# Kernel tuning notes

Measured on AMD Instinct MI355X. Metric: run time of the kernel, lower is better.

The kernel has to match this reference:

```python
import jax, jax.numpy as jnp
import numpy as np

ANCHORS = jnp.array([[0.57273, 0.677385], [1.87446, 2.06253], [3.33843, 5.47434],
                     [7.88282, 3.52778], [9.77052, 9.16828]], dtype=jnp.float32)
IOU_THR = 0.6
SCALE_NOOBJ = 1.0
SCALE_OBJ = 5.0
DS = 32.0          # downsample_rate
EPS = 1e-7


def _iou_wh(w1, h1, w2, h2):
    # GetCenterAlignIouBetween: boxes aligned at centers -> IoU depends on w,h only
    inter = jnp.minimum(w1, w2) * jnp.minimum(h1, h2)
    return inter / (w1 * h1 + w2 * h2 - inter + EPS)


def setup_inputs() -> dict:
    B, W, H, A, C, M = 128, 19, 19, 5, 81, 24
    N = W * H
    key = jax.random.key(0)
    ks = jax.random.split(key, 8)
    ii, jj = jnp.meshgrid(jnp.arange(W), jnp.arange(H), indexing='ij')
    fm_cord = jnp.stack([jj, ii], -1).reshape(N, 2).astype(jnp.float32)  # (x=j, y=i)
    conf = jax.random.uniform(ks[0], (B, W, H, A, 1)) * 0.98 + 0.01      # valid BCE probs
    pred_xy = fm_cord.reshape(1, W, H, 1, 2) + jax.random.uniform(ks[1], (B, W, H, A, 2))
    pred_wh = jax.random.uniform(ks[2], (B, W, H, A, 2)) * 8.0 + 0.2     # fm units, >0
    cls_score = jax.random.normal(ks[3], (B, W, H, A, C))
    # distinct grid cells per image so sequential scatter == vectorized scatter
    cells = jax.vmap(lambda k: jax.random.choice(k, N, (M,), replace=False))(
        jax.random.split(ks[4], B))
    ci = cells // H
    cj = cells % H
    frac = jax.random.uniform(ks[5], (B, M, 2))
    x = (cj.astype(jnp.float32) + frac[..., 0]) * DS   # pixel coords
    y = (ci.astype(jnp.float32) + frac[..., 1]) * DS
    wh = jax.random.uniform(ks[6], (B, M, 2), minval=12.0, maxval=280.0)
    true_object = jnp.stack([x, y, wh[..., 0], wh[..., 1]], -1)          # [B,M,4] pixels
    labels = jax.random.randint(ks[7], (B, M), 0, C - 1)
    true_label = jax.nn.one_hot(labels, C, dtype=jnp.float32)            # [B,M,C]
    return dict(epoch=0, conf=conf, pred_xy=pred_xy, pred_wh=pred_wh,
                cls_score=cls_score, true_label=true_label,
                true_object=true_object, fm_cord=fm_cord)


def _yolo_loss(conf, pred_xy, pred_wh, cls_score, true_label, true_object, fm_cord):
    B, W, H, A, C = cls_score.shape
    N = W * H
    NA = N * A
    S = float(W)  # config.output_size

    # ---- target assignment (vectorized version of the python loops) ----
    obj = true_object / DS                               # fm units, [B,M,4]
    gx, gy, gw, gh = obj[..., 0], obj[..., 1], obj[..., 2], obj[..., 3]
    i = gy.astype(jnp.int32)                             # row index  (int() truncation)
    j = gx.astype(jnp.int32)                             # col index
    cell = i * H + j                                     # flat cell, [B,M]

    a_iou = _iou_wh(ANCHORS[None, None, :, 0], ANCHORS[None, None, :, 1],
                    gw[..., None], gh[..., None])        # [B,M,A]
    best = jnp.argmax(a_iou, axis=-1)                    # [B,M]
    is_best = best[..., None] == jnp.arange(A)[None, None, :]
    over = a_iou > IOU_THR

    bb = jnp.arange(B)[:, None]
    pwh = pred_wh.reshape(B, N, A, 2)[bb, cell]          # [B,M,A,2] gather at gt cells
    pwh_b = jnp.take_along_axis(pwh, best[..., None, None], axis=2)[:, :, 0]  # [B,M,2]
    iou_pg = _iou_wh(pwh_b[..., 0], pwh_b[..., 1], gw, gh)                    # [B,M]

    mask_val = jnp.where(is_best, 1.0, jnp.where(over, -1.0, 0.0))            # [B,M,A]
    sw = 2.0 - (gw / S) * (gh / S)                                            # [B,M]
    sw_val = jnp.where(is_best, sw[..., None], jnp.where(over, -1.0, 0.0))
    pgi_val = jnp.where(~is_best & over, 0.0, iou_pg[..., None])              # [B,M,A]
    bg = jax.nn.one_hot(C - 1, C, dtype=cls_score.dtype)
    ts_val = jnp.where((is_best | over)[..., None], true_label[:, :, None, :], bg)
    bbox_val = jnp.where(is_best[..., None], obj[:, :, None, :], 0.0)         # [B,M,A,4]

    obj_mask = jnp.zeros((B, N, A)).at[bb, cell].set(mask_val)
    scale_w = jnp.zeros((B, N, A)).at[bb, cell].set(sw_val)
    pgi = jnp.zeros((B, N, A)).at[bb, cell].set(pgi_val)
    true_score = jnp.zeros((B, N, A, C)).at[..., -1].set(1.0).at[bb, cell].set(ts_val)
    true_bbox = jnp.zeros((B, N, A, 4)).at[bb, cell].set(bbox_val)

    # ---- masked losses over flattened [B, W*H*A, ...] ----
    conf_f = conf.reshape(B, NA)
    om = obj_mask.reshape(B, NA)
    swf = scale_w.reshape(B, NA)
    pgif = pgi.reshape(B, NA)
    pxy = pred_xy.reshape(B, NA, 2)
    pwh_f = pred_wh.reshape(B, NA, 2)
    tb = true_bbox.reshape(B, NA, 4)
    ts = true_score.reshape(B, NA, C)
    cs = cls_score.reshape(B, NA, C)
    cord = jnp.repeat(fm_cord[:, None, :], A, axis=1).reshape(NA, 2)

    cp = jnp.clip(conf_f, EPS, 1.0 - EPS)
    noobj_loss = SCALE_NOOBJ * jnp.sum((om == 0) * (-jnp.log(1.0 - cp))) / B
    obj_loss = SCALE_OBJ * jnp.sum(
        (om == 1) * (-(pgif * jnp.log(cp) + (1.0 - pgif) * jnp.log(1.0 - cp)))) / B

    gt = (swf > 0).astype(conf_f.dtype)                  # [B,NA]
    w3 = (SCALE_OBJ * gt * swf)[..., None]
    xy_loss = jnp.sum(w3 * ((pxy - cord[None]) - (tb[..., :2] - cord[None])) ** 2) / B
    wh_loss = jnp.sum(w3 * (pwh_f - tb[..., 2:]) ** 2) / B

    # CE with soft targets, per position: [B,NA]
    ce = -jnp.sum(ts * jax.nn.log_softmax(cs, axis=-1), axis=-1)
    # original broadcasts mask [B,1,NA] * ce [B,NA] -> [B,B,NA] then .sum();
    # equivalent factored form: sum_n (sum_b1 mask) * (sum_b2 ce)
    score_loss = SCALE_OBJ * jnp.sum(gt.sum(0) * ce.sum(0)) / B

    total = noobj_loss + obj_loss + xy_loss + wh_loss + score_loss
    return total, noobj_loss, obj_loss, score_loss, xy_loss, wh_loss


def reference(epoch, conf, pred_xy, pred_wh, cls_score, true_label, true_object, fm_cord):
    return _yolo_loss(conf, pred_xy, pred_wh, cls_score,
                      true_label, true_object, fm_cord)
```

## Files before the change

kernel.cpp:

```cpp
#include <hip/hip_runtime.h>

#define Bsz 128
#define Cd 81
#define Md 24
#define Nd 361
#define NAd 1805
#define TOTPOS 231040
#define RPW 16
#define NW_CLS (TOTPOS/RPW)
#define NOBJ (Bsz*Md)
#define NW_LAB (NOBJ/RPW)
#define EPSF 1e-7f
#define IOU_THRF 0.6f

#define OFF_CESUM 0
#define OFF_ACC   1808
#define OFF_GT    1824
#define OFF_NOOBJ 4096
#define OFF_LAB   20480
#define MEMSET_FLOATS 3629

__global__ __launch_bounds__(64) void yolo_sweep(
        const float* __restrict__ conf,
        const float* __restrict__ cls_score,
        const float* __restrict__ true_label,
        float* __restrict__ ws) {
    __shared__ float ex[RPW * Cd];
    const int bid = blockIdx.x;
    const int lane = threadIdx.x;
    const bool is_cls = bid < NW_CLS;

    const float* src = is_cls ? (cls_score + (size_t)bid * (RPW * Cd))
                              : (true_label + (size_t)(bid - NW_CLS) * (RPW * Cd));
    const float4* g = (const float4*)src;
    float4 r0 = g[0 * 64 + lane];
    float4 r1 = g[1 * 64 + lane];
    float4 r2 = g[2 * 64 + lane];
    float4 r3 = g[3 * 64 + lane];
    float4 r4 = g[4 * 64 + lane];
    float4 r5 = g[260 + lane];

    float nb = 0.0f;
    if (is_cls) {
        if (lane < RPW) {
            float cp = fminf(fmaxf(conf[bid * RPW + lane], EPSF), 1.0f - EPSF);
            nb = -__logf(1.0f - cp);
        }
        r0.x = __expf(r0.x); r0.y = __expf(r0.y); r0.z = __expf(r0.z); r0.w = __expf(r0.w);
        r1.x = __expf(r1.x); r1.y = __expf(r1.y); r1.z = __expf(r1.z); r1.w = __expf(r1.w);
        r2.x = __expf(r2.x); r2.y = __expf(r2.y); r2.z = __expf(r2.z); r2.w = __expf(r2.w);
        r3.x = __expf(r3.x); r3.y = __expf(r3.y); r3.z = __expf(r3.z); r3.w = __expf(r3.w);
        r4.x = __expf(r4.x); r4.y = __expf(r4.y); r4.z = __expf(r4.z); r4.w = __expf(r4.w);
        r5.x = __expf(r5.x); r5.y = __expf(r5.y); r5.z = __expf(r5.z); r5.w = __expf(r5.w);
    }
    float4* l4 = (float4*)ex;
    l4[0 * 64 + lane] = r0;
    l4[1 * 64 + lane] = r1;
    l4[2 * 64 + lane] = r2;
    l4[3 * 64 + lane] = r3;
    l4[4 * 64 + lane] = r4;
    l4[260 + lane] = r5;
    __syncthreads();

    const int r = lane >> 2, h = lane & 3;
    const float* p = ex + r * Cd;
    float s = 0.0f;
    #pragma unroll
    for (int j = 0; j < 21; j++) {
        int c = h * 21 + j;
        int cc = c < 81 ? c : 80;
        float w = (c < 81) ? (is_cls ? 1.0f : (float)c) : 0.0f;
        s += p[cc] * w;
    }
    s += __shfl_xor(s, 1, 64);
    s += __shfl_xor(s, 2, 64);

    if (h == 0) {
        int row = bid * RPW + r;
        if (is_cls) {
            float ce = __logf(s) - __logf(p[80]);
            int na = row % NAd;
            atomicAdd(&ws[OFF_CESUM + na], ce);
        } else {
            ws[OFF_LAB + ((bid - NW_CLS) * RPW + r)] = s;
        }
    }
    if (is_cls) {
        #pragma unroll
        for (int off = 32; off > 0; off >>= 1) nb += __shfl_xor(nb, off, 64);
        if (lane == 0) ws[OFF_NOOBJ + bid] = nb;
    }
}

__global__ __launch_bounds__(64) void yolo_assign(
        const float* __restrict__ conf,
        const float* __restrict__ pred_xy,
        const float* __restrict__ pred_wh,
        const float* __restrict__ cls_score,
        const float* __restrict__ true_object,
        float* __restrict__ ws) {
    const float AW[5] = {0.57273f, 1.87446f, 3.33843f, 7.88282f, 9.77052f};
    const float AH[5] = {0.677385f, 2.06253f, 5.47434f, 3.52778f, 9.16828f};
    const int idx = blockIdx.x * 64 + threadIdx.x;
    float* cesum = ws + OFF_CESUM;
    float* gt    = ws + OFF_GT;

    int lab = (int)(ws[OFF_LAB + idx] + 0.5f);
    int b = idx / Md;
    const float4 to = ((const float4*)true_object)[idx];
    const float inv_ds = 1.0f / 32.0f;
    float gx = to.x * inv_ds, gy = to.y * inv_ds;
    float gw = to.z * inv_ds, gh = to.w * inv_ds;
    int ci = (int)gy, cj = (int)gx;
    int cell = ci * 19 + cj;
    float garea = gw * gh;

    float best_iou = -1.0f; int best = 0; bool over[5];
    #pragma unroll
    for (int a = 0; a < 5; a++) {
        float inter = fminf(AW[a], gw) * fminf(AH[a], gh);
        float iou = inter / (AW[a] * AH[a] + garea - inter + EPSF);
        over[a] = iou > IOU_THRF;
        if (iou > best_iou) { best_iou = iou; best = a; }
    }

    int base_bn = (b * Nd + cell) * 5;
    float pwb = pred_wh[(size_t)(base_bn + best) * 2 + 0];
    float phb = pred_wh[(size_t)(base_bn + best) * 2 + 1];
    float inter = fminf(pwb, gw) * fminf(phb, gh);
    float iou_pg = inter / (pwb * phb + garea - inter + EPSF);
    float sw = 2.0f - (gw * (1.0f / 19.0f)) * (gh * (1.0f / 19.0f));

    float a0 = 0.f, a1 = 0.f, a2 = 0.f, a3 = 0.f;
    #pragma unroll
    for (int a = 0; a < 5; a++) {
        bool isb = (a == best);
        if (!(isb || over[a])) continue;
        int pos = base_bn + a;
        int na  = cell * 5 + a;
        float cp = fminf(fmaxf(conf[pos], EPSF), 1.0f - EPSF);
        a0 += __logf(1.0f - cp);
        const float* cs = cls_score + (size_t)pos * Cd;
        atomicAdd(&cesum[na], cs[Cd - 1] - cs[lab]);
        if (isb) {
            atomicAdd(&gt[na], 1.0f);
            a1 += -(iou_pg * __logf(cp) + (1.0f - iou_pg) * __logf(1.0f - cp));
            float px = pred_xy[(size_t)pos * 2 + 0], py = pred_xy[(size_t)pos * 2 + 1];
            a2 += sw * ((px - gx) * (px - gx) + (py - gy) * (py - gy));
            float pwa = pred_wh[(size_t)pos * 2 + 0], pha = pred_wh[(size_t)pos * 2 + 1];
            a3 += sw * ((pwa - gw) * (pwa - gw) + (pha - gh) * (pha - gh));
        }
    }

    #pragma unroll
    for (int off = 32; off > 0; off >>= 1) {
        a0 += __shfl_xor(a0, off, 64);
        a1 += __shfl_xor(a1, off, 64);
        a2 += __shfl_xor(a2, off, 64);
        a3 += __shfl_xor(a3, off, 64);
    }
    if (threadIdx.x == 0) {
        atomicAdd(&ws[OFF_ACC + 0], a0);
        atomicAdd(&ws[OFF_ACC + 1], a1);
        atomicAdd(&ws[OFF_ACC + 2], a2);
        atomicAdd(&ws[OFF_ACC + 3], a3);
    }
}

__global__ __launch_bounds__(1024) void yolo_reduce(
        const float* __restrict__ ws, float* __restrict__ out) {
    __shared__ float red[2][16];
    const int tid = threadIdx.x;
    float nsum = 0.0f;
    for (int i = tid; i < NW_CLS; i += 1024) nsum += ws[OFF_NOOBJ + i];
    float ssum = 0.0f;
    for (int na = tid; na < NAd; na += 1024)
        ssum += ws[OFF_GT + na] * ws[OFF_CESUM + na];

    float v[2] = {nsum, ssum};
    #pragma unroll
    for (int k = 0; k < 2; k++) {
        float x = v[k];
        #pragma unroll
        for (int off = 32; off > 0; off >>= 1) x += __shfl_xor(x, off, 64);
        if ((tid & 63) == 0) red[k][tid >> 6] = x;
    }
    __syncthreads();
    if (tid == 0) {
        float t0 = 0.f, t1 = 0.f;
        #pragma unroll
        for (int w = 0; w < 16; w++) { t0 += red[0][w]; t1 += red[1][w]; }
        const float invB = 1.0f / (float)Bsz;
        float noobj = 1.0f * (t0 + ws[OFF_ACC + 0]) * invB;
        float obj   = 5.0f * ws[OFF_ACC + 1] * invB;
        float xy    = 5.0f * ws[OFF_ACC + 2] * invB;
        float wh    = 5.0f * ws[OFF_ACC + 3] * invB;
        float score = 5.0f * t1 * invB;
        out[0] = noobj + obj + xy + wh + score;
        out[1] = noobj;
        out[2] = obj;
        out[3] = score;
        out[4] = xy;
        out[5] = wh;
    }
}

extern "C" void kernel_launch(void* const* d_in, const int* in_sizes, int n_in,
                              void* d_out, int out_size, void* d_ws, size_t ws_size,
                              hipStream_t stream) {
    const float* conf    = (const float*)d_in[1];
    const float* pred_xy = (const float*)d_in[2];
    const float* pred_wh = (const float*)d_in[3];
    const float* cls     = (const float*)d_in[4];
    const float* tlabel  = (const float*)d_in[5];
    const float* tobject = (const float*)d_in[6];
    float* ws  = (float*)d_ws;
    float* out = (float*)d_out;

    hipMemsetAsync(ws, 0, MEMSET_FLOATS * sizeof(float), stream);

    yolo_sweep<<<NW_CLS + NW_LAB, 64, 0, stream>>>(conf, cls, tlabel, ws);

    yolo_assign<<<NOBJ / 64, 64, 0, stream>>>(conf, pred_xy, pred_wh, cls, tobject, ws);

    yolo_reduce<<<1, 1024, 0, stream>>>(ws, out);
}
```

Baseline: 137.7 us.

## Make sweep kernel persistent with register prefetch of the next chunk

The sweep kernel now launches a fixed grid of 4096 single-wave blocks that grid-stride over all class-score and label chunks, instead of one block per chunk. Each iteration loads the next chunk's cls_score or true_label rows and conf values into registers while the current chunk is exponentiated, staged in LDS and reduced, so global-load latency overlaps compute. The block-wide __syncthreads becomes a wave barrier, which is valid because each block is one wave. The no-object partial sums are now accumulated per block across iterations, and the reduce kernel reads 4096 partials instead of one per chunk. The cost is higher register pressure from the double-buffered float4 loads.

```diff
diff --git a/kernel.cpp b/kernel.cpp
--- a/kernel.cpp
+++ b/kernel.cpp
@@ -7,9 +7,10 @@
 #define NAd 1805
 #define TOTPOS 231040
 #define RPW 16
-#define NW_CLS (TOTPOS/RPW)
+#define NCHUNK_CLS (TOTPOS/RPW)
 #define NOBJ (Bsz*Md)
-#define NW_LAB (NOBJ/RPW)
+#define NCHUNK_TOT (NCHUNK_CLS + NOBJ/RPW)
+#define NBLK 4096
 #define EPSF 1e-7f
 #define IOU_THRF 0.6f
 
@@ -20,76 +21,94 @@
 #define OFF_LAB   20480
 #define MEMSET_FLOATS 3629
 
+#define EXP4(v) { v.x=__expf(v.x); v.y=__expf(v.y); v.z=__expf(v.z); v.w=__expf(v.w); }
+
 __global__ __launch_bounds__(64) void yolo_sweep(
         const float* __restrict__ conf,
         const float* __restrict__ cls_score,
         const float* __restrict__ true_label,
         float* __restrict__ ws) {
     __shared__ float ex[RPW * Cd];
-    const int bid = blockIdx.x;
     const int lane = threadIdx.x;
-    const bool is_cls = bid < NW_CLS;
-
-    const float* src = is_cls ? (cls_score + (size_t)bid * (RPW * Cd))
-                              : (true_label + (size_t)(bid - NW_CLS) * (RPW * Cd));
-    const float4* g = (const float4*)src;
-    float4 r0 = g[0 * 64 + lane];
-    float4 r1 = g[1 * 64 + lane];
-    float4 r2 = g[2 * 64 + lane];
-    float4 r3 = g[3 * 64 + lane];
-    float4 r4 = g[4 * 64 + lane];
-    float4 r5 = g[260 + lane];
-
+    const int r = lane >> 2, h = lane & 3;
     float nb = 0.0f;
-    if (is_cls) {
-        if (lane < RPW) {
-            float cp = fminf(fmaxf(conf[bid * RPW + lane], EPSF), 1.0f - EPSF);
-            nb = -__logf(1.0f - cp);
-        }
-        r0.x = __expf(r0.x); r0.y = __expf(r0.y); r0.z = __expf(r0.z); r0.w = __expf(r0.w);
-        r1.x = __expf(r1.x); r1.y = __expf(r1.y); r1.z = __expf(r1.z); r1.w = __expf(r1.w);
-        r2.x = __expf(r2.x); r2.y = __expf(r2.y); r2.z = __expf(r2.z); r2.w = __expf(r2.w);
-        r3.x = __expf(r3.x); r3.y = __expf(r3.y); r3.z = __expf(r3.z); r3.w = __expf(r3.w);
-        r4.x = __expf(r4.x); r4.y = __expf(r4.y); r4.z = __expf(r4.z); r4.w = __expf(r4.w);
-        r5.x = __expf(r5.x); r5.y = __expf(r5.y); r5.z = __expf(r5.z); r5.w = __expf(r5.w);
-    }
-    float4* l4 = (float4*)ex;
-    l4[0 * 64 + lane] = r0;
-    l4[1 * 64 + lane] = r1;
-    l4[2 * 64 + lane] = r2;
-    l4[3 * 64 + lane] = r3;
-    l4[4 * 64 + lane] = r4;
-    l4[260 + lane] = r5;
-    __syncthreads();
-
-    const int r = lane >> 2, h = lane & 3;
-    const float* p = ex + r * Cd;
-    float s = 0.0f;
-    #pragma unroll
-    for (int j = 0; j < 21; j++) {
-        int c = h * 21 + j;
-        int cc = c < 81 ? c : 80;
-        float w = (c < 81) ? (is_cls ? 1.0f : (float)c) : 0.0f;
-        s += p[cc] * w;
-    }
-    s += __shfl_xor(s, 1, 64);
-    s += __shfl_xor(s, 2, 64);
-
-    if (h == 0) {
-        int row = bid * RPW + r;
+
+    int c = blockIdx.x;
+    {
+    }
+    const float4* g = (const float4*)(cls_score + (size_t)c * (RPW * Cd));
+    float4 u0 = g[0 * 64 + lane];
+    float4 u1 = g[1 * 64 + lane];
+    float4 u2 = g[2 * 64 + lane];
+    float4 u3 = g[3 * 64 + lane];
+    float4 u4 = g[4 * 64 + lane];
+    float4 u5 = g[260 + lane];
+    float cf = 0.0f;
+    if (lane < RPW) cf = conf[c * RPW + lane];
+
+    while (c < NCHUNK_TOT) {
+        const bool is_cls = c < NCHUNK_CLS;
+        if (is_cls) { EXP4(u0); EXP4(u1); EXP4(u2); EXP4(u3); EXP4(u4); EXP4(u5); }
+        float4* l4 = (float4*)ex;
+        l4[0 * 64 + lane] = u0;
+        l4[1 * 64 + lane] = u1;
+        l4[2 * 64 + lane] = u2;
+        l4[3 * 64 + lane] = u3;
+        l4[4 * 64 + lane] = u4;
+        l4[260 + lane] = u5;
+        __builtin_amdgcn_wave_barrier();
+
+        const int cn = c + NBLK;
+        float4 n0 = {}, n1 = {}, n2 = {}, n3 = {}, n4 = {}, n5 = {};
+        float cfn = 0.0f;
+        if (cn < NCHUNK_TOT) {
+            const float* srcn = (cn < NCHUNK_CLS)
+                ? (cls_score + (size_t)cn * (RPW * Cd))
+                : (true_label + (size_t)(cn - NCHUNK_CLS) * (RPW * Cd));
+            const float4* gn = (const float4*)srcn;
+            n0 = gn[0 * 64 + lane];
+            n1 = gn[1 * 64 + lane];
+            n2 = gn[2 * 64 + lane];
+            n3 = gn[3 * 64 + lane];
+            n4 = gn[4 * 64 + lane];
+            n5 = gn[260 + lane];
+            if (cn < NCHUNK_CLS && lane < RPW) cfn = conf[cn * RPW + lane];
+        }
+
+        const float* p = ex + r * Cd;
+        float s = 0.0f;
+        #pragma unroll
+        for (int j = 0; j < 21; j++) {
+            int c0 = h * 21 + j;
+            int cc = c0 < 81 ? c0 : 80;
+            float w = (c0 < 81) ? (is_cls ? 1.0f : (float)c0) : 0.0f;
+            s += p[cc] * w;
+        }
+        s += __shfl_xor(s, 1, 64);
+        s += __shfl_xor(s, 2, 64);
+
         if (is_cls) {
-            float ce = __logf(s) - __logf(p[80]);
-            int na = row % NAd;
-            atomicAdd(&ws[OFF_CESUM + na], ce);
+            if (lane < RPW) {
+                float cp = fminf(fmaxf(cf, EPSF), 1.0f - EPSF);
+                nb += -__logf(1.0f - cp);
+            }
+            if (h == 0) {
+                int row = c * RPW + r;
+                int na = row % NAd;
+                float ce = __logf(s) - __logf(p[80]);
+                atomicAdd(&ws[OFF_CESUM + na], ce);
+            }
         } else {
-            ws[OFF_LAB + ((bid - NW_CLS) * RPW + r)] = s;
-        }
-    }
-    if (is_cls) {
-        #pragma unroll
-        for (int off = 32; off > 0; off >>= 1) nb += __shfl_xor(nb, off, 64);
-        if (lane == 0) ws[OFF_NOOBJ + bid] = nb;
-    }
+            if (h == 0) ws[OFF_LAB + ((c - NCHUNK_CLS) * RPW + r)] = s;
+        }
+
+        u0 = n0; u1 = n1; u2 = n2; u3 = n3; u4 = n4; u5 = n5; cf = cfn;
+        c = cn;
+    }
+
+    #pragma unroll
+    for (int off = 32; off > 0; off >>= 1) nb += __shfl_xor(nb, off, 64);
+    if (lane == 0) ws[OFF_NOOBJ + blockIdx.x] = nb;
 }
 
 __global__ __launch_bounds__(64) void yolo_assign(
@@ -172,7 +191,7 @@
     __shared__ float red[2][16];
     const int tid = threadIdx.x;
     float nsum = 0.0f;
-    for (int i = tid; i < NW_CLS; i += 1024) nsum += ws[OFF_NOOBJ + i];
+    for (int i = tid; i < NBLK; i += 1024) nsum += ws[OFF_NOOBJ + i];
     float ssum = 0.0f;
     for (int na = tid; na < NAd; na += 1024)
         ssum += ws[OFF_GT + na] * ws[OFF_CESUM + na];
@@ -219,7 +238,7 @@
 
     hipMemsetAsync(ws, 0, MEMSET_FLOATS * sizeof(float), stream);
 
-    yolo_sweep<<<NW_CLS + NW_LAB, 64, 0, stream>>>(conf, cls, tlabel, ws);
+    yolo_sweep<<<NBLK, 64, 0, stream>>>(conf, cls, tlabel, ws);
 
     yolo_assign<<<NOBJ / 64, 64, 0, stream>>>(conf, pred_xy, pred_wh, cls, tobject, ws);
 
```

New measurement: 135.3 us. About the same (-1.8%).
